# Kernel optimization log

Hardware: AMD Instinct MI355X
Metric: run time of the kernel (lower is better)

The kernel has to match this reference:

```python
import jax, jax.numpy as jnp
import numpy as np

N = 50000
E = 800000
IN_DIM = 128
OUT_DIM = 128


def setup_inputs() -> dict:
    key = jax.random.key(0)
    k1, k2, k3, k4 = jax.random.split(key, 4)
    x = jax.random.normal(k1, (N, IN_DIM), dtype=jnp.float32)
    edge_index = jax.random.randint(k2, (2, E), 0, N, dtype=jnp.int64)
    # Linear(in_dim*2, out_dim) params
    W = jax.random.normal(k3, (2 * IN_DIM, OUT_DIM), dtype=jnp.float32) * (1.0 / np.sqrt(2 * IN_DIM))
    b = jax.random.normal(k4, (OUT_DIM,), dtype=jnp.float32) * 0.01
    return {"x": x, "edge_index": edge_index, "W": W, "b": b}


def reference(x, edge_index, W, b):
    src, dst = edge_index[0], edge_index[1]
    diff = x[src] - x[dst]                              # (E, C)
    # segment-max over destination nodes; empty segments get -inf identity
    seg_max = jax.ops.segment_max(diff, dst, num_segments=N)  # (N, C)
    counts = jax.ops.segment_sum(jnp.ones((E,), dtype=jnp.int32), dst, num_segments=N)
    # original code leaves zeros for nodes with no incoming edges
    max_diff = jnp.where((counts > 0)[:, None], seg_max, jnp.zeros_like(seg_max))
    x_cat = jnp.concatenate([x, max_diff], axis=-1)     # (N, 2C)
    return x_cat @ W + b
```

## Files before the change

### kernel.cpp

```cpp
#include <hip/hip_runtime.h>
#include <math.h>

#define NN 50000
#define NE 800000
#define CD 128
#define PB 3200
#define OVCAP 65536

typedef __attribute__((ext_vector_type(8))) short short8;
typedef __attribute__((ext_vector_type(4))) float f32x4;


__device__ inline unsigned pack2bf(float lo, float hi) {
    unsigned a = __float_as_uint(lo), b = __float_as_uint(hi);
    a = (a + 0x7fffu + ((a >> 16) & 1u)) >> 16;
    b = (b + 0x7fffu + ((b >> 16) & 1u)) & 0xffff0000u;
    return a | b;
}

__device__ inline unsigned short f2bf(float f) {
    unsigned u = __float_as_uint(f);
    return (unsigned short)((u + 0x7fffu + ((u >> 16) & 1u)) >> 16);
}

__device__ inline void fmax8(float* m, uint4 v) {
    m[0] = fmaxf(m[0], __uint_as_float(v.x << 16));
    m[1] = fmaxf(m[1], __uint_as_float(v.x & 0xffff0000u));
    m[2] = fmaxf(m[2], __uint_as_float(v.y << 16));
    m[3] = fmaxf(m[3], __uint_as_float(v.y & 0xffff0000u));
    m[4] = fmaxf(m[4], __uint_as_float(v.z << 16));
    m[5] = fmaxf(m[5], __uint_as_float(v.z & 0xffff0000u));
    m[6] = fmaxf(m[6], __uint_as_float(v.w << 16));
    m[7] = fmaxf(m[7], __uint_as_float(v.w & 0xffff0000u));
}


__global__ __launch_bounds__(256) void prep_k(const int* __restrict__ ei,
                                              const float* __restrict__ x,
                                              const float* __restrict__ W,
                                              int* __restrict__ cnt,
                                              unsigned short* __restrict__ bkt,
                                              unsigned* __restrict__ ovl,
                                              unsigned* __restrict__ xb,
                                              unsigned short* __restrict__ wt) {
    int tid0 = blockIdx.x * 256 + threadIdx.x;
    int phase = blockIdx.x & 1;

    for (int p = 0; p < 2; p++) {
        if ((p ^ phase) == 0) {
            for (int e = tid0; e < NE; e += PB * 256) {
                int s = ei[e];
                int d = ei[NE + e];
                int k = atomicAdd(&cnt[d], 1);
                if (k < 64) {
                    bkt[(size_t)d * 64 + k] = (unsigned short)s;
                } else {
                    unsigned oi = atomicAdd((unsigned*)&cnt[NN], 1u);
                    if (oi < OVCAP) ovl[oi] = ((unsigned)d << 16) | (unsigned)s;
                }
            }
        } else {
            for (int i = tid0; i < NN * CD / 4; i += PB * 256) {
                float4 v = ((const float4*)x)[i];
                uint2 r;
                r.x = pack2bf(v.x, v.y);
                r.y = pack2bf(v.z, v.w);
                ((uint2*)xb)[i] = r;
            }
        }
    }
    for (int i = tid0; i < 2 * CD * CD; i += PB * 256) {
        int n = i >> 8, k = i & 255;
        wt[(size_t)n * 256 + k] = f2bf(W[(size_t)k * 128 + n]);
    }
}


__global__ __launch_bounds__(128) void gather_k(const unsigned* __restrict__ xb,
                                                const int* __restrict__ cnt,
                                                const unsigned short* __restrict__ bkt,
                                                const unsigned* __restrict__ ovl,
                                                unsigned* __restrict__ outu) {
    int t = threadIdx.x;
    int q = t >> 4, c = t & 15;
    int node = blockIdx.x * 8 + q;
    int cntv = cnt[node];
    int cn = min(cntv, 64);
    const unsigned short* brow = bkt + (size_t)node * 64;

    float m[8];
#pragma unroll
    for (int i = 0; i < 8; i++) m[i] = -INFINITY;

    for (int base = 0; base < cn; base += 8) {
        uint4 pk = *(const uint4*)(brow + base);
        int s0 = (int)(pk.x & 0xffffu), s1 = (int)(pk.x >> 16);
        int s2 = (int)(pk.y & 0xffffu), s3 = (int)(pk.y >> 16);
        int s4 = (int)(pk.z & 0xffffu), s5 = (int)(pk.z >> 16);
        int s6 = (int)(pk.w & 0xffffu), s7 = (int)(pk.w >> 16);
        if (base + 8 <= cn) {
            fmax8(m, *(const uint4*)(xb + (size_t)s0 * 64 + c * 4));
            fmax8(m, *(const uint4*)(xb + (size_t)s1 * 64 + c * 4));
            fmax8(m, *(const uint4*)(xb + (size_t)s2 * 64 + c * 4));
            fmax8(m, *(const uint4*)(xb + (size_t)s3 * 64 + c * 4));
            fmax8(m, *(const uint4*)(xb + (size_t)s4 * 64 + c * 4));
            fmax8(m, *(const uint4*)(xb + (size_t)s5 * 64 + c * 4));
            fmax8(m, *(const uint4*)(xb + (size_t)s6 * 64 + c * 4));
            fmax8(m, *(const uint4*)(xb + (size_t)s7 * 64 + c * 4));
        } else {
            if (base + 0 < cn) fmax8(m, *(const uint4*)(xb + (size_t)s0 * 64 + c * 4));
            if (base + 1 < cn) fmax8(m, *(const uint4*)(xb + (size_t)s1 * 64 + c * 4));
            if (base + 2 < cn) fmax8(m, *(const uint4*)(xb + (size_t)s2 * 64 + c * 4));
            if (base + 3 < cn) fmax8(m, *(const uint4*)(xb + (size_t)s3 * 64 + c * 4));
            if (base + 4 < cn) fmax8(m, *(const uint4*)(xb + (size_t)s4 * 64 + c * 4));
            if (base + 5 < cn) fmax8(m, *(const uint4*)(xb + (size_t)s5 * 64 + c * 4));
            if (base + 6 < cn) fmax8(m, *(const uint4*)(xb + (size_t)s6 * 64 + c * 4));
            if (base + 7 < cn) fmax8(m, *(const uint4*)(xb + (size_t)s7 * 64 + c * 4));
        }
    }
    if (cntv > 64) {
        unsigned no = (unsigned)cnt[NN];
        if (no > OVCAP) no = OVCAP;
        for (unsigned i2 = 0; i2 < no; i2++) {
            unsigned u = ovl[i2];
            if ((int)(u >> 16) == node)
                fmax8(m, *(const uint4*)(xb + (size_t)(u & 0xffffu) * 64 + c * 4));
        }
    }
    uint4 r = make_uint4(0u, 0u, 0u, 0u);
    if (cntv > 0) {
        uint4 xd = *(const uint4*)(xb + (size_t)node * 64 + c * 4);
        float d0 = m[0] - __uint_as_float(xd.x << 16);
        float d1 = m[1] - __uint_as_float(xd.x & 0xffff0000u);
        float d2 = m[2] - __uint_as_float(xd.y << 16);
        float d3 = m[3] - __uint_as_float(xd.y & 0xffff0000u);
        float d4 = m[4] - __uint_as_float(xd.z << 16);
        float d5 = m[5] - __uint_as_float(xd.z & 0xffff0000u);
        float d6 = m[6] - __uint_as_float(xd.w << 16);
        float d7 = m[7] - __uint_as_float(xd.w & 0xffff0000u);
        r.x = pack2bf(d0, d1);
        r.y = pack2bf(d2, d3);
        r.z = pack2bf(d4, d5);
        r.w = pack2bf(d6, d7);
    }
    *(uint4*)(outu + (size_t)node * 128 + 64 + c * 4) = r;
}


__global__ __launch_bounds__(256) void gemm_k(const unsigned* __restrict__ xb,
                                              const unsigned* __restrict__ amxu,
                                              const short* __restrict__ wt,
                                              const float* __restrict__ bias,
                                              float* __restrict__ out) {
    int t = threadIdx.x;
    int w = t >> 6, lane = t & 63;
    int mm = lane & 15, g = lane >> 4;
    int rt = w & 1, ch = w >> 1;
    int nbase = blockIdx.x * 32;
    int r0 = nbase + rt * 16;
    int row = r0 + mm;
    bool rowok = row < NN;

    uint4 afr[8];
#pragma unroll
    for (int kc = 0; kc < 4; kc++)
        afr[kc] = rowok ? *(const uint4*)(xb + (size_t)row * 64 + kc * 16 + g * 4)
                        : make_uint4(0u, 0u, 0u, 0u);
#pragma unroll
    for (int kc = 4; kc < 8; kc++)
        afr[kc] = rowok ? *(const uint4*)(amxu + (size_t)row * 128 + 64 + (kc - 4) * 16 + g * 4)
                        : make_uint4(0u, 0u, 0u, 0u);

    __syncthreads();

    f32x4 acc[4];
#pragma unroll
    for (int ct = 0; ct < 4; ct++) {
        float bv = bias[ch * 64 + ct * 16 + mm];
        acc[ct] = (f32x4){bv, bv, bv, bv};
    }

#pragma unroll
    for (int kc = 0; kc < 8; kc++) {
        short8 a;
        __builtin_memcpy(&a, &afr[kc], 16);
#pragma unroll
        for (int ct = 0; ct < 4; ct++) {
            short8 b = *(const short8*)(wt + (size_t)(ch * 64 + ct * 16 + mm) * 256 + kc * 32 + g * 8);
            acc[ct] = __builtin_amdgcn_mfma_f32_16x16x32_bf16(a, b, acc[ct], 0, 0, 0);
        }
    }

#pragma unroll
    for (int ct = 0; ct < 4; ct++) {
#pragma unroll
        for (int i = 0; i < 4; i++) {
            int rr = r0 + g * 4 + i;
            if (rr < NN) out[(size_t)rr * 128 + ch * 64 + ct * 16 + mm] = acc[ct][i];
        }
    }
}


extern "C" void kernel_launch(void* const* d_in, const int* in_sizes, int n_in,
                              void* d_out, int out_size, void* d_ws, size_t ws_size,
                              hipStream_t stream) {
    const float* x = (const float*)d_in[0];
    const int* ei = (const int*)d_in[1];
    const float* W = (const float*)d_in[2];
    const float* bias = (const float*)d_in[3];
    float* out = (float*)d_out;

    int* wsi = (int*)d_ws;
    int* cnt = wsi;
    unsigned short* bkt = (unsigned short*)(wsi + 50016);
    unsigned* xb = (unsigned*)(wsi + 1650016);
    unsigned short* wt = (unsigned short*)(wsi + 4850016);
    unsigned* ovl = (unsigned*)(wsi + 4866400);

    hipMemsetAsync(cnt, 0, 50016 * sizeof(int), stream);

    prep_k<<<PB, 256, 0, stream>>>(ei, x, W, cnt, bkt, ovl, xb, wt);
    gather_k<<<NN / 8, 128, 0, stream>>>(xb, cnt, bkt, ovl, (unsigned*)out);
    gemm_k<<<(NN + 31) / 32, 256, 0, stream>>>(xb, (const unsigned*)out, (const short*)wt,
                                               bias, out);
}
```

Baseline: 189.5 us.

## Split bf16 features into channel-quarter planes and gather per plane

Result: slower. 214.4 us (+13.1%).

```diff
diff --git a/kernel.cpp b/kernel.cpp
--- a/kernel.cpp
+++ b/kernel.cpp
@@ -4,7 +4,7 @@
 #define NN 50000
 #define NE 800000
 #define CD 128
-#define PB 3200
+#define BSL 32
 #define OVCAP 65536
 
 typedef __attribute__((ext_vector_type(8))) short short8;
@@ -23,55 +23,47 @@
     return (unsigned short)((u + 0x7fffu + ((u >> 16) & 1u)) >> 16);
 }
 
-__device__ inline void fmax8(float* m, uint4 v) {
-    m[0] = fmaxf(m[0], __uint_as_float(v.x << 16));
-    m[1] = fmaxf(m[1], __uint_as_float(v.x & 0xffff0000u));
-    m[2] = fmaxf(m[2], __uint_as_float(v.y << 16));
-    m[3] = fmaxf(m[3], __uint_as_float(v.y & 0xffff0000u));
-    m[4] = fmaxf(m[4], __uint_as_float(v.z << 16));
-    m[5] = fmaxf(m[5], __uint_as_float(v.z & 0xffff0000u));
-    m[6] = fmaxf(m[6], __uint_as_float(v.w << 16));
-    m[7] = fmaxf(m[7], __uint_as_float(v.w & 0xffff0000u));
-}
-
-
-__global__ __launch_bounds__(256) void prep_k(const int* __restrict__ ei,
-                                              const float* __restrict__ x,
+__device__ inline void fmax2(float* m, unsigned v) {
+    m[0] = fmaxf(m[0], __uint_as_float(v << 16));
+    m[1] = fmaxf(m[1], __uint_as_float(v & 0xffff0000u));
+}
+
+
+__global__ __launch_bounds__(256) void scatter_k(const int* __restrict__ ei,
+                                                 int* __restrict__ cnt,
+                                                 unsigned short* __restrict__ bkt,
+                                                 unsigned* __restrict__ ovl) {
+    int e = blockIdx.x * 256 + threadIdx.x;
+    int s = ei[e];
+    int d = ei[NE + e];
+    int k = atomicAdd(&cnt[d], 1);
+    if (k < BSL) {
+        bkt[(size_t)d * BSL + k] = (unsigned short)s;
+    } else {
+        unsigned oi = atomicAdd((unsigned*)&cnt[NN], 1u);
+        if (oi < OVCAP) ovl[oi] = ((unsigned)d << 16) | (unsigned)s;
+    }
+}
+
+
+__global__ __launch_bounds__(256) void cast_k(const float* __restrict__ x,
                                               const float* __restrict__ W,
-                                              int* __restrict__ cnt,
-                                              unsigned short* __restrict__ bkt,
-                                              unsigned* __restrict__ ovl,
                                               unsigned* __restrict__ xb,
                                               unsigned short* __restrict__ wt) {
-    int tid0 = blockIdx.x * 256 + threadIdx.x;
-    int phase = blockIdx.x & 1;
-
-    for (int p = 0; p < 2; p++) {
-        if ((p ^ phase) == 0) {
-            for (int e = tid0; e < NE; e += PB * 256) {
-                int s = ei[e];
-                int d = ei[NE + e];
-                int k = atomicAdd(&cnt[d], 1);
-                if (k < 64) {
-                    bkt[(size_t)d * 64 + k] = (unsigned short)s;
-                } else {
-                    unsigned oi = atomicAdd((unsigned*)&cnt[NN], 1u);
-                    if (oi < OVCAP) ovl[oi] = ((unsigned)d << 16) | (unsigned)s;
-                }
-            }
-        } else {
-            for (int i = tid0; i < NN * CD / 4; i += PB * 256) {
-                float4 v = ((const float4*)x)[i];
-                uint2 r;
-                r.x = pack2bf(v.x, v.y);
-                r.y = pack2bf(v.z, v.w);
-                ((uint2*)xb)[i] = r;
-            }
-        }
-    }
-    for (int i = tid0; i < 2 * CD * CD; i += PB * 256) {
-        int n = i >> 8, k = i & 255;
-        wt[(size_t)n * 256 + k] = f2bf(W[(size_t)k * 128 + n]);
+    int i = blockIdx.x * 256 + threadIdx.x;
+    int n = i >> 4, r = i & 15, q = r >> 2, j = r & 3;
+    const float4* xr = (const float4*)(x + (size_t)n * 128 + q * 32 + j * 8);
+    float4 a = xr[0], b = xr[1];
+    uint4 o;
+    o.x = pack2bf(a.x, a.y);
+    o.y = pack2bf(a.z, a.w);
+    o.z = pack2bf(b.x, b.y);
+    o.w = pack2bf(b.z, b.w);
+    *(uint4*)(xb + (size_t)q * (NN * 16) + (size_t)n * 16 + j * 4) = o;
+
+    if (i < 2 * CD * CD) {
+        int nn = i >> 8, k = i & 255;
+        wt[(size_t)nn * 256 + k] = f2bf(W[(size_t)k * 128 + nn]);
     }
 }
 
@@ -81,16 +73,18 @@
                                                 const unsigned short* __restrict__ bkt,
                                                 const unsigned* __restrict__ ovl,
                                                 unsigned* __restrict__ outu) {
-    int t = threadIdx.x;
-    int q = t >> 4, c = t & 15;
-    int node = blockIdx.x * 8 + q;
+    int b = blockIdx.x;
+    int q = (b & 7) >> 1;
+    int t = ((b >> 3) << 1) | (b & 1);
+    int node = t * 8 + (threadIdx.x >> 4);
+    int c = threadIdx.x & 15;
+    const unsigned* plane = xb + (size_t)q * (NN * 16);
+
     int cntv = cnt[node];
-    int cn = min(cntv, 64);
-    const unsigned short* brow = bkt + (size_t)node * 64;
-
-    float m[8];
-#pragma unroll
-    for (int i = 0; i < 8; i++) m[i] = -INFINITY;
+    int cn = min(cntv, BSL);
+    const unsigned short* brow = bkt + (size_t)node * BSL;
+
+    float m[2] = {-INFINITY, -INFINITY};
 
     for (int base = 0; base < cn; base += 8) {
         uint4 pk = *(const uint4*)(brow + base);
@@ -99,51 +93,42 @@
         int s4 = (int)(pk.z & 0xffffu), s5 = (int)(pk.z >> 16);
         int s6 = (int)(pk.w & 0xffffu), s7 = (int)(pk.w >> 16);
         if (base + 8 <= cn) {
-            fmax8(m, *(const uint4*)(xb + (size_t)s0 * 64 + c * 4));
-            fmax8(m, *(const uint4*)(xb + (size_t)s1 * 64 + c * 4));
-            fmax8(m, *(const uint4*)(xb + (size_t)s2 * 64 + c * 4));
-            fmax8(m, *(const uint4*)(xb + (size_t)s3 * 64 + c * 4));
-            fmax8(m, *(const uint4*)(xb + (size_t)s4 * 64 + c * 4));
-            fmax8(m, *(const uint4*)(xb + (size_t)s5 * 64 + c * 4));
-            fmax8(m, *(const uint4*)(xb + (size_t)s6 * 64 + c * 4));
-            fmax8(m, *(const uint4*)(xb + (size_t)s7 * 64 + c * 4));
+            fmax2(m, plane[(size_t)s0 * 16 + c]);
+            fmax2(m, plane[(size_t)s1 * 16 + c]);
+            fmax2(m, plane[(size_t)s2 * 16 + c]);
+            fmax2(m, plane[(size_t)s3 * 16 + c]);
+            fmax2(m, plane[(size_t)s4 * 16 + c]);
+            fmax2(m, plane[(size_t)s5 * 16 + c]);
+            fmax2(m, plane[(size_t)s6 * 16 + c]);
+            fmax2(m, plane[(size_t)s7 * 16 + c]);
         } else {
-            if (base + 0 < cn) fmax8(m, *(const uint4*)(xb + (size_t)s0 * 64 + c * 4));
-            if (base + 1 < cn) fmax8(m, *(const uint4*)(xb + (size_t)s1 * 64 + c * 4));
-            if (base + 2 < cn) fmax8(m, *(const uint4*)(xb + (size_t)s2 * 64 + c * 4));
-            if (base + 3 < cn) fmax8(m, *(const uint4*)(xb + (size_t)s3 * 64 + c * 4));
-            if (base + 4 < cn) fmax8(m, *(const uint4*)(xb + (size_t)s4 * 64 + c * 4));
-            if (base + 5 < cn) fmax8(m, *(const uint4*)(xb + (size_t)s5 * 64 + c * 4));
-            if (base + 6 < cn) fmax8(m, *(const uint4*)(xb + (size_t)s6 * 64 + c * 4));
-            if (base + 7 < cn) fmax8(m, *(const uint4*)(xb + (size_t)s7 * 64 + c * 4));
-        }
-    }
-    if (cntv > 64) {
+            if (base + 0 < cn) fmax2(m, plane[(size_t)s0 * 16 + c]);
+            if (base + 1 < cn) fmax2(m, plane[(size_t)s1 * 16 + c]);
+            if (base + 2 < cn) fmax2(m, plane[(size_t)s2 * 16 + c]);
+            if (base + 3 < cn) fmax2(m, plane[(size_t)s3 * 16 + c]);
+            if (base + 4 < cn) fmax2(m, plane[(size_t)s4 * 16 + c]);
+            if (base + 5 < cn) fmax2(m, plane[(size_t)s5 * 16 + c]);
+            if (base + 6 < cn) fmax2(m, plane[(size_t)s6 * 16 + c]);
+            if (base + 7 < cn) fmax2(m, plane[(size_t)s7 * 16 + c]);
+        }
+    }
+    if (cntv > BSL) {
         unsigned no = (unsigned)cnt[NN];
         if (no > OVCAP) no = OVCAP;
         for (unsigned i2 = 0; i2 < no; i2++) {
             unsigned u = ovl[i2];
             if ((int)(u >> 16) == node)
-                fmax8(m, *(const uint4*)(xb + (size_t)(u & 0xffffu) * 64 + c * 4));
-        }
-    }
-    uint4 r = make_uint4(0u, 0u, 0u, 0u);
+                fmax2(m, plane[(size_t)(u & 0xffffu) * 16 + c]);
+        }
+    }
+    unsigned r = 0u;
     if (cntv > 0) {
-        uint4 xd = *(const uint4*)(xb + (size_t)node * 64 + c * 4);
-        float d0 = m[0] - __uint_as_float(xd.x << 16);
-        float d1 = m[1] - __uint_as_float(xd.x & 0xffff0000u);
-        float d2 = m[2] - __uint_as_float(xd.y << 16);
-        float d3 = m[3] - __uint_as_float(xd.y & 0xffff0000u);
-        float d4 = m[4] - __uint_as_float(xd.z << 16);
-        float d5 = m[5] - __uint_as_float(xd.z & 0xffff0000u);
-        float d6 = m[6] - __uint_as_float(xd.w << 16);
-        float d7 = m[7] - __uint_as_float(xd.w & 0xffff0000u);
-        r.x = pack2bf(d0, d1);
-        r.y = pack2bf(d2, d3);
-        r.z = pack2bf(d4, d5);
-        r.w = pack2bf(d6, d7);
-    }
-    *(uint4*)(outu + (size_t)node * 128 + 64 + c * 4) = r;
+        unsigned xd = plane[(size_t)node * 16 + c];
+        float d0 = m[0] - __uint_as_float(xd << 16);
+        float d1 = m[1] - __uint_as_float(xd & 0xffff0000u);
+        r = pack2bf(d0, d1);
+    }
+    outu[(size_t)node * 128 + 64 + q * 16 + c] = r;
 }
 
 
@@ -164,7 +149,7 @@
     uint4 afr[8];
 #pragma unroll
     for (int kc = 0; kc < 4; kc++)
-        afr[kc] = rowok ? *(const uint4*)(xb + (size_t)row * 64 + kc * 16 + g * 4)
+        afr[kc] = rowok ? *(const uint4*)(xb + (size_t)kc * (NN * 16) + (size_t)row * 16 + g * 4)
                         : make_uint4(0u, 0u, 0u, 0u);
 #pragma unroll
     for (int kc = 4; kc < 8; kc++)
@@ -214,14 +199,15 @@
     int* wsi = (int*)d_ws;
     int* cnt = wsi;
     unsigned short* bkt = (unsigned short*)(wsi + 50016);
-    unsigned* xb = (unsigned*)(wsi + 1650016);
-    unsigned short* wt = (unsigned short*)(wsi + 4850016);
-    unsigned* ovl = (unsigned*)(wsi + 4866400);
+    unsigned* xb = (unsigned*)(wsi + 850016);
+    unsigned short* wt = (unsigned short*)(wsi + 4050016);
+    unsigned* ovl = (unsigned*)(wsi + 4066400);
 
     hipMemsetAsync(cnt, 0, 50016 * sizeof(int), stream);
 
-    prep_k<<<PB, 256, 0, stream>>>(ei, x, W, cnt, bkt, ovl, xb, wt);
-    gather_k<<<NN / 8, 128, 0, stream>>>(xb, cnt, bkt, ovl, (unsigned*)out);
+    scatter_k<<<NE / 256, 256, 0, stream>>>(ei, cnt, bkt, ovl);
+    cast_k<<<NN * 16 / 256, 256, 0, stream>>>(x, W, xb, wt);
+    gather_k<<<25000, 128, 0, stream>>>(xb, cnt, bkt, ovl, (unsigned*)out);
     gemm_k<<<(NN + 31) / 32, 256, 0, stream>>>(xb, (const unsigned*)out, (const short*)wt,
                                                bias, out);
 }
```

## Split bf16 features into column-quarter planes and slice bucketing by destination range

Applied to the files above, without the earlier changes.

Result: slower. 193.5 us (+2.1%).

```diff
diff --git a/kernel.cpp b/kernel.cpp
--- a/kernel.cpp
+++ b/kernel.cpp
@@ -4,11 +4,16 @@
 #define NN 50000
 #define NE 800000
 #define CD 128
-#define PB 3200
+#define BSL 32
 #define OVCAP 65536
+#define SB 125
+#define CHK (NE / SB)
+#define SLICE (NN / 8)
+#define PGRID (8 * SB * 256)
 
 typedef __attribute__((ext_vector_type(8))) short short8;
 typedef __attribute__((ext_vector_type(4))) float f32x4;
+typedef __attribute__((ext_vector_type(4))) unsigned uint4v;
 
 
 __device__ inline unsigned pack2bf(float lo, float hi) {
@@ -44,32 +49,51 @@
                                               unsigned* __restrict__ xb,
                                               unsigned short* __restrict__ wt) {
     int tid0 = blockIdx.x * 256 + threadIdx.x;
-    int phase = blockIdx.x & 1;
+    int slice = blockIdx.x & 7;
+    int chunk = blockIdx.x >> 3;
+    int phase = chunk & 1;
 
     for (int p = 0; p < 2; p++) {
         if ((p ^ phase) == 0) {
-            for (int e = tid0; e < NE; e += PB * 256) {
-                int s = ei[e];
-                int d = ei[NE + e];
-                int k = atomicAdd(&cnt[d], 1);
-                if (k < 64) {
-                    bkt[(size_t)d * 64 + k] = (unsigned short)s;
-                } else {
-                    unsigned oi = atomicAdd((unsigned*)&cnt[NN], 1u);
-                    if (oi < OVCAP) ovl[oi] = ((unsigned)d << 16) | (unsigned)s;
+            int lo = slice * SLICE;
+            int e0 = chunk * CHK;
+            const int* dsts = ei + NE;
+            for (int e = e0 + threadIdx.x; e < e0 + CHK; e += 256) {
+                int d = __builtin_nontemporal_load(dsts + e);
+                if ((unsigned)(d - lo) < (unsigned)SLICE) {
+                    int s = __builtin_nontemporal_load(ei + e);
+                    int k = atomicAdd(&cnt[d], 1);
+                    if (k < BSL) {
+                        bkt[(size_t)d * BSL + k] = (unsigned short)s;
+                    } else {
+                        unsigned oi = atomicAdd((unsigned*)&cnt[NN], 1u);
+                        if (oi < OVCAP) ovl[oi] = ((unsigned)d << 16) | (unsigned)s;
+                    }
                 }
             }
         } else {
-            for (int i = tid0; i < NN * CD / 4; i += PB * 256) {
-                float4 v = ((const float4*)x)[i];
-                uint2 r;
-                r.x = pack2bf(v.x, v.y);
-                r.y = pack2bf(v.z, v.w);
-                ((uint2*)xb)[i] = r;
+            for (int i = tid0; i < NN * 16; i += PGRID) {
+                int n = i >> 4, r = i & 15, q = r >> 2, j = r & 3;
+                const float* xr = x + (size_t)n * 128 + q * 32 + j * 8;
+                float4 a, b;
+                a.x = __builtin_nontemporal_load(xr + 0);
+                a.y = __builtin_nontemporal_load(xr + 1);
+                a.z = __builtin_nontemporal_load(xr + 2);
+                a.w = __builtin_nontemporal_load(xr + 3);
+                b.x = __builtin_nontemporal_load(xr + 4);
+                b.y = __builtin_nontemporal_load(xr + 5);
+                b.z = __builtin_nontemporal_load(xr + 6);
+                b.w = __builtin_nontemporal_load(xr + 7);
+                uint4v o;
+                o.x = pack2bf(a.x, a.y);
+                o.y = pack2bf(a.z, a.w);
+                o.z = pack2bf(b.x, b.y);
+                o.w = pack2bf(b.z, b.w);
+                __builtin_nontemporal_store(o, (uint4v*)(xb + (size_t)q * (NN * 16) + (size_t)n * 16 + j * 4));
             }
         }
     }
-    for (int i = tid0; i < 2 * CD * CD; i += PB * 256) {
+    for (int i = tid0; i < 2 * CD * CD; i += PGRID) {
         int n = i >> 8, k = i & 255;
         wt[(size_t)n * 256 + k] = f2bf(W[(size_t)k * 128 + n]);
     }
@@ -81,12 +105,16 @@
                                                 const unsigned short* __restrict__ bkt,
                                                 const unsigned* __restrict__ ovl,
                                                 unsigned* __restrict__ outu) {
-    int t = threadIdx.x;
-    int q = t >> 4, c = t & 15;
-    int node = blockIdx.x * 8 + q;
-    int cntv = cnt[node];
-    int cn = min(cntv, 64);
-    const unsigned short* brow = bkt + (size_t)node * 64;
+    int b = blockIdx.x;
+    int q = (b & 7) >> 1;
+    int t = ((b >> 3) << 1) | (b & 1);
+    int node = t * 32 + (threadIdx.x >> 2);
+    int j = threadIdx.x & 3;
+    const unsigned* plane = xb + (size_t)q * (NN * 16);
+
+    int cntv = (node < NN) ? cnt[node] : 0;
+    int cn = min(cntv, BSL);
+    const unsigned short* brow = bkt + (size_t)node * BSL;
 
     float m[8];
 #pragma unroll
@@ -99,37 +127,37 @@
         int s4 = (int)(pk.z & 0xffffu), s5 = (int)(pk.z >> 16);
         int s6 = (int)(pk.w & 0xffffu), s7 = (int)(pk.w >> 16);
         if (base + 8 <= cn) {
-            fmax8(m, *(const uint4*)(xb + (size_t)s0 * 64 + c * 4));
-            fmax8(m, *(const uint4*)(xb + (size_t)s1 * 64 + c * 4));
-            fmax8(m, *(const uint4*)(xb + (size_t)s2 * 64 + c * 4));
-            fmax8(m, *(const uint4*)(xb + (size_t)s3 * 64 + c * 4));
-            fmax8(m, *(const uint4*)(xb + (size_t)s4 * 64 + c * 4));
-            fmax8(m, *(const uint4*)(xb + (size_t)s5 * 64 + c * 4));
-            fmax8(m, *(const uint4*)(xb + (size_t)s6 * 64 + c * 4));
-            fmax8(m, *(const uint4*)(xb + (size_t)s7 * 64 + c * 4));
+            fmax8(m, *(const uint4*)(plane + (size_t)s0 * 16 + j * 4));
+            fmax8(m, *(const uint4*)(plane + (size_t)s1 * 16 + j * 4));
+            fmax8(m, *(const uint4*)(plane + (size_t)s2 * 16 + j * 4));
+            fmax8(m, *(const uint4*)(plane + (size_t)s3 * 16 + j * 4));
+            fmax8(m, *(const uint4*)(plane + (size_t)s4 * 16 + j * 4));
+            fmax8(m, *(const uint4*)(plane + (size_t)s5 * 16 + j * 4));
+            fmax8(m, *(const uint4*)(plane + (size_t)s6 * 16 + j * 4));
+            fmax8(m, *(const uint4*)(plane + (size_t)s7 * 16 + j * 4));
         } else {
-            if (base + 0 < cn) fmax8(m, *(const uint4*)(xb + (size_t)s0 * 64 + c * 4));
-            if (base + 1 < cn) fmax8(m, *(const uint4*)(xb + (size_t)s1 * 64 + c * 4));
-            if (base + 2 < cn) fmax8(m, *(const uint4*)(xb + (size_t)s2 * 64 + c * 4));
-            if (base + 3 < cn) fmax8(m, *(const uint4*)(xb + (size_t)s3 * 64 + c * 4));
-            if (base + 4 < cn) fmax8(m, *(const uint4*)(xb + (size_t)s4 * 64 + c * 4));
-            if (base + 5 < cn) fmax8(m, *(const uint4*)(xb + (size_t)s5 * 64 + c * 4));
-            if (base + 6 < cn) fmax8(m, *(const uint4*)(xb + (size_t)s6 * 64 + c * 4));
-            if (base + 7 < cn) fmax8(m, *(const uint4*)(xb + (size_t)s7 * 64 + c * 4));
-        }
-    }
-    if (cntv > 64) {
+            if (base + 0 < cn) fmax8(m, *(const uint4*)(plane + (size_t)s0 * 16 + j * 4));
+            if (base + 1 < cn) fmax8(m, *(const uint4*)(plane + (size_t)s1 * 16 + j * 4));
+            if (base + 2 < cn) fmax8(m, *(const uint4*)(plane + (size_t)s2 * 16 + j * 4));
+            if (base + 3 < cn) fmax8(m, *(const uint4*)(plane + (size_t)s3 * 16 + j * 4));
+            if (base + 4 < cn) fmax8(m, *(const uint4*)(plane + (size_t)s4 * 16 + j * 4));
+            if (base + 5 < cn) fmax8(m, *(const uint4*)(plane + (size_t)s5 * 16 + j * 4));
+            if (base + 6 < cn) fmax8(m, *(const uint4*)(plane + (size_t)s6 * 16 + j * 4));
+            if (base + 7 < cn) fmax8(m, *(const uint4*)(plane + (size_t)s7 * 16 + j * 4));
+        }
+    }
+    if (cntv > BSL) {
         unsigned no = (unsigned)cnt[NN];
         if (no > OVCAP) no = OVCAP;
         for (unsigned i2 = 0; i2 < no; i2++) {
             unsigned u = ovl[i2];
             if ((int)(u >> 16) == node)
-                fmax8(m, *(const uint4*)(xb + (size_t)(u & 0xffffu) * 64 + c * 4));
+                fmax8(m, *(const uint4*)(plane + (size_t)(u & 0xffffu) * 16 + j * 4));
         }
     }
     uint4 r = make_uint4(0u, 0u, 0u, 0u);
     if (cntv > 0) {
-        uint4 xd = *(const uint4*)(xb + (size_t)node * 64 + c * 4);
+        uint4 xd = *(const uint4*)(plane + (size_t)node * 16 + j * 4);
         float d0 = m[0] - __uint_as_float(xd.x << 16);
         float d1 = m[1] - __uint_as_float(xd.x & 0xffff0000u);
         float d2 = m[2] - __uint_as_float(xd.y << 16);
@@ -143,7 +171,8 @@
         r.z = pack2bf(d4, d5);
         r.w = pack2bf(d6, d7);
     }
-    *(uint4*)(outu + (size_t)node * 128 + 64 + c * 4) = r;
+    if (node < NN)
+        *(uint4*)(outu + (size_t)node * 128 + 64 + q * 16 + j * 4) = r;
 }
 
 
@@ -164,7 +193,7 @@
     uint4 afr[8];
 #pragma unroll
     for (int kc = 0; kc < 4; kc++)
-        afr[kc] = rowok ? *(const uint4*)(xb + (size_t)row * 64 + kc * 16 + g * 4)
+        afr[kc] = rowok ? *(const uint4*)(xb + (size_t)kc * (NN * 16) + (size_t)row * 16 + g * 4)
                         : make_uint4(0u, 0u, 0u, 0u);
 #pragma unroll
     for (int kc = 4; kc < 8; kc++)
@@ -214,14 +243,14 @@
     int* wsi = (int*)d_ws;
     int* cnt = wsi;
     unsigned short* bkt = (unsigned short*)(wsi + 50016);
-    unsigned* xb = (unsigned*)(wsi + 1650016);
-    unsigned short* wt = (unsigned short*)(wsi + 4850016);
-    unsigned* ovl = (unsigned*)(wsi + 4866400);
-
-    hipMemsetAsync(cnt, 0, 50016 * sizeof(int), stream);
-
-    prep_k<<<PB, 256, 0, stream>>>(ei, x, W, cnt, bkt, ovl, xb, wt);
-    gather_k<<<NN / 8, 128, 0, stream>>>(xb, cnt, bkt, ovl, (unsigned*)out);
+    unsigned* xb = (unsigned*)(wsi + 850016);
+    unsigned short* wt = (unsigned short*)(wsi + 4050016);
+    unsigned* ovl = (unsigned*)(wsi + 4066400);
+
+    (void)hipMemsetAsync(cnt, 0, 50016 * sizeof(int), stream);
+
+    prep_k<<<8 * SB, 256, 0, stream>>>(ei, x, W, cnt, bkt, ovl, xb, wt);
+    gather_k<<<6256, 128, 0, stream>>>(xb, cnt, bkt, ovl, (unsigned*)out);
     gemm_k<<<(NN + 31) / 32, 256, 0, stream>>>(xb, (const unsigned*)out, (const short*)wt,
                                                bias, out);
 }
```
